# Kernel optimization log

Measured on AMD Instinct MI355X. Metric: run time of the kernel, lower is better.

Reference implementation:

```python
import jax, jax.numpy as jnp
import numpy as np

D_MODEL = 1024
N_HEADS = 16
D_K = D_MODEL // N_HEADS  # 64
SCALE = 0.125             # attention_scale = 1/sqrt(d_k)
ROPE_BASE = 10000.0
NEG_INF = -1e30


def setup_inputs() -> dict:
    key = jax.random.key(0)
    k1, k2, k3 = jax.random.split(key, 3)
    B, S = 2, 2048
    x = jax.random.normal(k1, (B, S, D_MODEL), jnp.float32)
    # torch Linear(d_model, 3*d_model, bias=False): stored here as [in, out]
    w_qkv = jax.random.normal(k2, (D_MODEL, 3 * D_MODEL), jnp.float32) * (D_MODEL ** -0.5)
    w_o = jax.random.normal(k3, (D_MODEL, D_MODEL), jnp.float32) * (D_MODEL ** -0.5)
    return {"x": x, "w_qkv": w_qkv, "w_o": w_o}


def _rotary(x):
    # x: [B, H, S, D]; standard half-split rotary over sequence positions
    S, D = x.shape[2], x.shape[3]
    inv_freq = 1.0 / (ROPE_BASE ** (jnp.arange(0, D, 2, dtype=jnp.float32) / D))  # [D/2]
    freqs = jnp.arange(S, dtype=jnp.float32)[:, None] * inv_freq[None, :]          # [S, D/2]
    cos = jnp.cos(freqs)[None, None]  # [1,1,S,D/2]
    sin = jnp.sin(freqs)[None, None]
    x1, x2 = jnp.split(x, 2, axis=-1)
    return jnp.concatenate([x1 * cos + x2 * sin, -x1 * sin + x2 * cos], axis=-1).astype(x.dtype)


def reference(x, w_qkv, w_o):
    B, S, _ = x.shape
    qkv = x @ w_qkv                                        # [B,S,3*D_MODEL]
    qkv = qkv.reshape(B, S, 3, N_HEADS, D_K).transpose(2, 0, 3, 1, 4)  # [3,B,H,S,Dk]
    q, k, v = qkv[0], qkv[1], qkv[2]
    q = _rotary(q)
    k = _rotary(k)
    scores = jnp.einsum('bhqd,bhkd->bhqk', q, k) * SCALE   # [B,H,S,S]
    causal = jnp.tril(jnp.ones((S, S), dtype=bool))
    scores = jnp.where(causal, scores, NEG_INF)
    attn = jax.nn.softmax(scores, axis=-1)
    out = jnp.einsum('bhqk,bhkd->bhqd', attn, v)           # [B,H,S,Dk]
    out = out.transpose(0, 2, 1, 3).reshape(B, S, D_MODEL)
    return out @ w_o
```

## Files before the change

### kernel.cpp

```cpp
#include <hip/hip_runtime.h>

typedef short bf16x8 __attribute__((ext_vector_type(8)));
typedef short bf16x4 __attribute__((ext_vector_type(4)));
typedef float f32x4 __attribute__((ext_vector_type(4)));
typedef float f32x16 __attribute__((ext_vector_type(16)));
typedef int i32x4 __attribute__((ext_vector_type(4)));

#define DEVI static __device__ __forceinline__

DEVI unsigned short f2b(float f) {
  unsigned u = __float_as_uint(f);
  u += 0x7FFFu + ((u >> 16) & 1u);
  return (unsigned short)(u >> 16);
}

DEVI void gload16(const void* g, void* l) {
  __builtin_amdgcn_global_load_lds((const __attribute__((address_space(1))) void*)g,
                                   (__attribute__((address_space(3))) void*)l, 16, 0, 0);
}

DEVI void pl32swap(int a, int b, int& outa, int& outb) {
#if __has_builtin(__builtin_amdgcn_permlane32_swap)
  auto r = __builtin_amdgcn_permlane32_swap(a, b, false, false);
  outa = ((const int*)&r)[0];
  outb = ((const int*)&r)[1];
#else
  int bp = __shfl_xor(b, 32);
  int ap = __shfl_xor(a, 32);
  outa = (threadIdx.x & 32) ? bp : a;
  outb = (threadIdx.x & 32) ? b : ap;
#endif
}

DEVI float halfmax(float x) {
  int o0, o1;
  pl32swap(__float_as_int(x), __float_as_int(x), o0, o1);
  return fmaxf(__int_as_float(o0), __int_as_float(o1));
}
DEVI float halfsum(float x) {
  int o0, o1;
  pl32swap(__float_as_int(x), __float_as_int(x), o0, o1);
  return __int_as_float(o0) + __int_as_float(o1);
}

__global__ void rope_table_kernel(float2* __restrict__ cst) {
  int i = blockIdx.x * 256 + threadIdx.x;
  int s = i >> 5, j = i & 31;
  float inv = powf(10000.0f, -(float)j * (1.0f / 32.0f));
  float a = (float)s * inv;
  cst[i] = make_float2(cosf(a), sinf(a));
}

__global__ void cvt_x_kernel(const float* __restrict__ x, unsigned short* __restrict__ xb) {
  int i = blockIdx.x * 256 + threadIdx.x;
  float4 v = ((const float4*)x)[i];
  ushort4 o;
  o.x = f2b(v.x); o.y = f2b(v.y); o.z = f2b(v.z); o.w = f2b(v.w);
  ((ushort4*)xb)[i] = o;
}

__global__ void transpose_kernel(const float* __restrict__ W, unsigned short* __restrict__ WT,
                                 int K, int N) {
  __shared__ float tile[32][33];
  int n0 = blockIdx.x * 32, k0 = blockIdx.y * 32;
  int tx = threadIdx.x, ty = threadIdx.y;
#pragma unroll
  for (int i = 0; i < 32; i += 8)
    tile[ty + i][tx] = W[(size_t)(k0 + ty + i) * N + n0 + tx];
  __syncthreads();
#pragma unroll
  for (int i = 0; i < 32; i += 8)
    WT[(size_t)(n0 + ty + i) * K + k0 + tx] = f2b(tile[tx][ty + i]);
}

__global__ __launch_bounds__(512, 2) void gemm_qkv_kernel(
    const unsigned short* __restrict__ Xb, const unsigned short* __restrict__ WT,
    const float2* __restrict__ cst,
    unsigned short* __restrict__ Qb, unsigned short* __restrict__ Kb,
    unsigned short* __restrict__ VTb) {
  __shared__ unsigned short As[2][256 * 64];
  __shared__ unsigned short Bs[2][256 * 64];
  const int tid = threadIdx.x;
  const int lane = tid & 63, wid = tid >> 6;
  const int flat = blockIdx.y * 12 + blockIdx.x;
  const int nf = (flat & 7) * 24 + (flat >> 3);
  const int bx = nf % 12, by = nf / 12;
  const int m0 = by * 256, n0 = bx * 256;
  const int wr = wid >> 2, wc = wid & 3;
  const int srow = lane >> 3;
  const int scc = ((lane & 7) ^ srow) * 8;
  const int rx = lane & 7;

  f32x4 acc[8][4] = {};

  auto stageA = [&](int k0, int nb, int i) {
    const int c = i * 8 + wid;
    const int row = c * 8 + srow;
    gload16(Xb + (size_t)(m0 + row) * 1024 + k0 + scc, (char*)As[nb] + c * 1024);
  };
  auto stageB = [&](int k0, int nb, int i) {
    const int c = i * 8 + wid;
    const int row = c * 8 + srow;
    gload16(WT + (size_t)(n0 + row) * 1024 + k0 + scc, (char*)Bs[nb] + c * 1024);
  };
  auto loadA = [&](const unsigned short* Ab, int q, bf16x8 af[2][2]) {
#pragma unroll
    for (int kk = 0; kk < 2; ++kk) {
      const int cc = ((kk * 4 + (lane >> 4)) ^ rx) * 8;
#pragma unroll
      for (int miL = 0; miL < 2; ++miL)
        af[miL][kk] = *(const bf16x8*)&Ab[(wr * 128 + (q * 2 + miL) * 16 + (lane & 15)) * 64 + cc];
    }
  };

#define QKV_MFMA_QUAD(Q)                                                      \
  __builtin_amdgcn_s_barrier();                                               \
  asm volatile("s_waitcnt lgkmcnt(0)" ::: "memory");                          \
  __builtin_amdgcn_s_setprio(1);                                              \
  _Pragma("unroll") for (int kk = 0; kk < 2; ++kk)                            \
    _Pragma("unroll") for (int miL = 0; miL < 2; ++miL)                       \
      _Pragma("unroll") for (int ni = 0; ni < 4; ++ni)                        \
        acc[(Q) * 2 + miL][ni] = __builtin_amdgcn_mfma_f32_16x16x32_bf16(     \
            af[miL][kk], bf[ni][kk], acc[(Q) * 2 + miL][ni], 0, 0, 0);        \
  __builtin_amdgcn_s_setprio(0);                                              \
  __builtin_amdgcn_s_barrier();

#pragma unroll
  for (int i = 0; i < 4; ++i) stageB(0, 0, i);
#pragma unroll
  for (int i = 0; i < 4; ++i) stageA(0, 0, i);
#pragma unroll
  for (int i = 0; i < 4; ++i) stageB(64, 1, i);
  stageA(64, 1, 0); stageA(64, 1, 2);
  asm volatile("s_waitcnt vmcnt(6)" ::: "memory");
  __builtin_amdgcn_s_barrier();

  for (int t = 0; t < 16; ++t) {
    const int b = t & 1;
    const unsigned short* Ab = As[b];
    const unsigned short* Bb = Bs[b];
    const int k1 = (t + 1) * 64, k2 = (t + 2) * 64;
    bf16x8 bf[4][2], af[2][2];

#pragma unroll
    for (int kk = 0; kk < 2; ++kk) {
      const int cc = ((kk * 4 + (lane >> 4)) ^ rx) * 8;
#pragma unroll
      for (int ni = 0; ni < 4; ++ni)
        bf[ni][kk] = *(const bf16x8*)&Bb[(wc * 64 + ni * 16 + (lane & 15)) * 64 + cc];
    }
    loadA(Ab, 0, af);
    if (t + 1 < 16) { stageA(k1, b ^ 1, 1); stageA(k1, b ^ 1, 3); }
    QKV_MFMA_QUAD(0)

    loadA(Ab, 1, af);
    if (t + 2 < 16) { stageB(k2, b, 0); stageB(k2, b, 1); }
    QKV_MFMA_QUAD(1)

    loadA(Ab, 2, af);
    if (t + 2 < 16) { stageB(k2, b, 2); stageB(k2, b, 3); }
    QKV_MFMA_QUAD(2)

    loadA(Ab, 3, af);
    if (t + 2 < 16) { stageA(k2, b, 0); stageA(k2, b, 2); }
    __builtin_amdgcn_s_barrier();
    asm volatile("s_waitcnt lgkmcnt(0)" ::: "memory");
    __builtin_amdgcn_s_setprio(1);
#pragma unroll
    for (int kk = 0; kk < 2; ++kk)
#pragma unroll
      for (int miL = 0; miL < 2; ++miL)
#pragma unroll
        for (int ni = 0; ni < 4; ++ni)
          acc[6 + miL][ni] = __builtin_amdgcn_mfma_f32_16x16x32_bf16(
              af[miL][kk], bf[ni][kk], acc[6 + miL][ni], 0, 0, 0);
    __builtin_amdgcn_s_setprio(0);
    if (t + 2 < 16) asm volatile("s_waitcnt vmcnt(6)" ::: "memory");
    else            asm volatile("s_waitcnt vmcnt(0)" ::: "memory");
    __builtin_amdgcn_s_barrier();
  }
#undef QKV_MFMA_QUAD

  unsigned short* slab = (wid < 4) ? (&As[0][0] + wid * 8192)
                                   : (&Bs[0][0] + (wid - 4) * 8192);
  const int n_base = n0 + wc * 64;
  const int ty = n_base >> 10;
  const int h = (n_base & 1023) >> 6;
  const int qrow = (lane >> 4) << 2;
  const int l15 = lane & 15;
  const int rlane = lane >> 3, clane = lane & 7;

  if (ty < 2) {
    unsigned short* dst = (ty == 0) ? Qb : Kb;
#pragma unroll
    for (int g = 0; g < 2; ++g) {
      const int rowg = m0 + wr * 128 + g * 64;
      const int s_half = rowg & 2047, bb = rowg >> 11;
#pragma unroll
      for (int miL = 0; miL < 4; ++miL) {
        const int mi = g * 4 + miL;
        const int rl0 = miL * 16 + qrow;
#pragma unroll
        for (int r = 0; r < 4; ++r) {
#pragma unroll
          for (int ni = 0; ni < 2; ++ni) {
            const int j = ni * 16 + l15;
            const float2 cs = cst[(s_half + rl0 + r) * 32 + j];
            const float x1 = acc[mi][ni][r], x2 = acc[mi][ni + 2][r];
            slab[(rl0 + r) * 72 + j]      = f2b(x1 * cs.x + x2 * cs.y);
            slab[(rl0 + r) * 72 + j + 32] = f2b(-x1 * cs.y + x2 * cs.x);
          }
        }
      }
      unsigned short* dp = dst + ((size_t)(bb * 16 + h) * 2048 + s_half) * 64;
#pragma unroll
      for (int i = 0; i < 8; ++i) {
        const int row = i * 8 + rlane;
        const bf16x8 v = *(const bf16x8*)&slab[row * 72 + clane * 8];
        *(bf16x8*)&dp[row * 64 + clane * 8] = v;
      }
    }
  } else {
#pragma unroll
    for (int g = 0; g < 2; ++g) {
      const int rowg = m0 + wr * 128 + g * 64;
      const int s_half = rowg & 2047, bb = rowg >> 11;
#pragma unroll
      for (int miL = 0; miL < 4; ++miL) {
        const int mi = g * 4 + miL;
        const int rl0 = miL * 16 + qrow;
#pragma unroll
        for (int ni = 0; ni < 4; ++ni) {
          const int d = ni * 16 + l15;
#pragma unroll
          for (int r = 0; r < 4; ++r)
            slab[d * 72 + rl0 + r] = f2b(acc[mi][ni][r]);
        }
      }
      unsigned short* vp = VTb + (size_t)(bb * 16 + h) * 64 * 2048 + s_half;
#pragma unroll
      for (int i = 0; i < 8; ++i) {
        const int d = i * 8 + rlane;
        const bf16x8 v = *(const bf16x8*)&slab[d * 72 + clane * 8];
        *(bf16x8*)&vp[(size_t)d * 2048 + clane * 8] = v;
      }
    }
  }
}

DEVI void gemm_mainloop(const unsigned short* __restrict__ A, const unsigned short* __restrict__ B,
                        unsigned short* As, unsigned short* Bs,
                        int m0, int n0, int lane, int wid, int wr, int wc,
                        f32x4 acc[4][4]) {
  const int srow = lane >> 3;
  const int scc = ((lane & 7) ^ srow) * 8;
  const int rx = lane & 7;
  auto stage = [&](int k0, int nb) {
    unsigned short* Ad = As + nb * 8192;
    unsigned short* Bd = Bs + nb * 8192;
#pragma unroll
    for (int i = 0; i < 4; ++i) {
      const int c = i * 4 + wid;
      const int row = c * 8 + srow;
      gload16(A + (size_t)(m0 + row) * 1024 + k0 + scc, (char*)Ad + c * 1024);
      gload16(B + (size_t)(n0 + row) * 1024 + k0 + scc, (char*)Bd + c * 1024);
    }
  };
  auto compute = [&](int nb) {
    const unsigned short* Ab = As + nb * 8192;
    const unsigned short* Bb = Bs + nb * 8192;
#pragma unroll
    for (int kk = 0; kk < 64; kk += 32) {
      const int cc = (((kk >> 3) + (lane >> 4)) ^ rx) * 8;
      bf16x8 a[4], b[4];
#pragma unroll
      for (int mi = 0; mi < 4; ++mi)
        a[mi] = *(const bf16x8*)&Ab[(wr * 64 + mi * 16 + (lane & 15)) * 64 + cc];
#pragma unroll
      for (int ni = 0; ni < 4; ++ni)
        b[ni] = *(const bf16x8*)&Bb[(wc * 64 + ni * 16 + (lane & 15)) * 64 + cc];
      __builtin_amdgcn_s_setprio(1);
#pragma unroll
      for (int mi = 0; mi < 4; ++mi)
#pragma unroll
        for (int ni = 0; ni < 4; ++ni)
          acc[mi][ni] = __builtin_amdgcn_mfma_f32_16x16x32_bf16(a[mi], b[ni], acc[mi][ni], 0, 0, 0);
      __builtin_amdgcn_s_setprio(0);
    }
  };
  stage(0, 0);
  stage(64, 1);
  for (int t = 0; t < 15; ++t) {
    asm volatile("s_waitcnt vmcnt(8)" ::: "memory");
    __builtin_amdgcn_s_barrier();
    compute(t & 1);
    __builtin_amdgcn_s_barrier();
    if (t < 14) stage((t + 2) * 64, t & 1);
  }
  asm volatile("s_waitcnt vmcnt(0)" ::: "memory");
  __builtin_amdgcn_s_barrier();
  compute(1);
}

DEVI void stage256(const unsigned short* __restrict__ Kh, const unsigned short* __restrict__ Vh,
                   int kbase, unsigned char* buf, int tid) {
#pragma unroll
  for (int i = 0; i < 4; ++i) {
    const int T = tid + i * 1024;
    const int g = T >> 10;
    const int rem = T & 1023;
    const int rr = (rem & 511) >> 3, c = rem & 7, cc = c ^ (rr & 7);
    unsigned char* dst = buf + (T & ~63) * 16;
    if (rem < 512)
      gload16(Kh + (size_t)(kbase + g * 64 + rr) * 64 + cc * 8, dst);
    else
      gload16(Vh + (size_t)rr * 2048 + kbase + g * 64 + cc * 8, dst);
  }
}

DEVI void attn_sub(const unsigned char* __restrict__ bufK, const unsigned char* __restrict__ bufV,
                   const bf16x8 qf[4], int s32, int kglob, bool diag, int qg, int ln, int hi,
                   float& m2, float& l_run, f32x16& acc0, f32x16& acc1) {
  const float C = 0.125f * 1.44269504f;
  const int rx = ln & 7;
  bf16x8 kf[4];
#pragma unroll
  for (int j = 0; j < 4; ++j) {
    const int cc = (2 * j + hi) ^ rx;
    kf[j] = *(const bf16x8*)(bufK + (s32 * 32 + ln) * 128 + cc * 16);
  }
  bf16x8 v0[2], v1[2];
#pragma unroll
  for (int p = 0; p < 2; ++p) {
    const int cc = (4 * s32 + 2 * p + hi) ^ rx;
    v0[p] = *(const bf16x8*)(bufV + ln * 128 + cc * 16);
    v1[p] = *(const bf16x8*)(bufV + (ln + 32) * 128 + cc * 16);
  }

  f32x16 stv = {};
  __builtin_amdgcn_s_setprio(1);
  stv = __builtin_amdgcn_mfma_f32_32x32x16_bf16(kf[0], qf[0], stv, 0, 0, 0);
  stv = __builtin_amdgcn_mfma_f32_32x32x16_bf16(kf[1], qf[1], stv, 0, 0, 0);
  stv = __builtin_amdgcn_mfma_f32_32x32x16_bf16(kf[2], qf[2], stv, 0, 0, 0);
  stv = __builtin_amdgcn_mfma_f32_32x32x16_bf16(kf[3], qf[3], stv, 0, 0, 0);
  __builtin_amdgcn_s_setprio(0);

  float sraw[16];
#pragma unroll
  for (int r = 0; r < 16; ++r) sraw[r] = stv[r];
  if (diag) {
#pragma unroll
    for (int r = 0; r < 16; ++r) {
      const int kg = kglob + (r & 3) + ((r >> 2) << 3) + (hi << 2);
      if (kg > qg) sraw[r] = -1e30f;
    }
  }
  float mraw = sraw[0];
#pragma unroll
  for (int r = 1; r < 16; ++r) mraw = fmaxf(mraw, sraw[r]);
  const float mlc = mraw * C;
  if (__any(mlc > m2 + 11.5416f)) {
    const float mnew = fmaxf(m2, halfmax(mlc));
    const float sc = exp2f(m2 - mnew);
    l_run *= sc;
#pragma unroll
    for (int r = 0; r < 16; ++r) { acc0[r] *= sc; acc1[r] *= sc; }
    m2 = mnew;
  }
  float p[16], ps = 0.f;
#pragma unroll
  for (int r = 0; r < 16; ++r) { p[r] = exp2f(fmaf(sraw[r], C, -m2)); ps += p[r]; }
  l_run += ps;

  int cw[8];
#pragma unroll
  for (int i = 0; i < 8; ++i)
    asm("v_cvt_pk_bf16_f32 %0, %1, %2" : "=v"(cw[i]) : "v"(p[2 * i]), "v"(p[2 * i + 1]));
  int a0, a1, b0, b1, a2, a3, b2, b3;
  pl32swap(cw[0], cw[2], a0, b0);
  pl32swap(cw[1], cw[3], a1, b1);
  pl32swap(cw[4], cw[6], a2, b2);
  pl32swap(cw[5], cw[7], a3, b3);
  const bf16x8 pa0 = __builtin_bit_cast(bf16x8, (i32x4){a0, a1, b0, b1});
  const bf16x8 pa1 = __builtin_bit_cast(bf16x8, (i32x4){a2, a3, b2, b3});

  __builtin_amdgcn_s_setprio(1);
  acc0 = __builtin_amdgcn_mfma_f32_32x32x16_bf16(v0[0], pa0, acc0, 0, 0, 0);
  acc0 = __builtin_amdgcn_mfma_f32_32x32x16_bf16(v0[1], pa1, acc0, 0, 0, 0);
  acc1 = __builtin_amdgcn_mfma_f32_32x32x16_bf16(v1[0], pa0, acc1, 0, 0, 0);
  acc1 = __builtin_amdgcn_mfma_f32_32x32x16_bf16(v1[1], pa1, acc1, 0, 0, 0);
  __builtin_amdgcn_s_setprio(0);
}

DEVI void write_partial(float* M, int slot, const f32x16& a0, const f32x16& a1,
                        float m2, float l) {
#pragma unroll
  for (int r = 0; r < 16; ++r) { M[slot + r] = a0[r]; M[slot + 16 + r] = a1[r]; }
  M[slot + 32] = m2;
  M[slot + 33] = l;
}

DEVI void merge_state(const float* M, int slot, float& m, float& l,
                      f32x16& a0, f32x16& a1) {
  const float mp = M[slot + 32], lp = M[slot + 33];
  const float mn = fmaxf(m, mp);
  const float eo = exp2f(m - mn), ep = exp2f(mp - mn);
  l = l * eo + lp * ep;
#pragma unroll
  for (int r = 0; r < 16; ++r) {
    a0[r] = a0[r] * eo + M[slot + r] * ep;
    a1[r] = a1[r] * eo + M[slot + 16 + r] * ep;
  }
  m = mn;
}

DEVI void writeO(unsigned short* __restrict__ Ob, const f32x16& a0, const f32x16& a1,
                 float l, int bh, int q0, int ln, int hi) {
  const float il = 1.0f / l;
  const int b = bh >> 4, h = bh & 15;
  unsigned short* ob = Ob + ((size_t)(b * 2048 + q0 + ln)) * 1024 + h * 64;
#pragma unroll
  for (int g = 0; g < 4; ++g) {
    ushort4 o0, o1;
    o0.x = f2b(a0[4 * g + 0] * il); o0.y = f2b(a0[4 * g + 1] * il);
    o0.z = f2b(a0[4 * g + 2] * il); o0.w = f2b(a0[4 * g + 3] * il);
    o1.x = f2b(a1[4 * g + 0] * il); o1.y = f2b(a1[4 * g + 1] * il);
    o1.z = f2b(a1[4 * g + 2] * il); o1.w = f2b(a1[4 * g + 3] * il);
    *(ushort4*)&ob[8 * g + 4 * hi]      = o0;
    *(ushort4*)&ob[32 + 8 * g + 4 * hi] = o1;
  }
}

__global__ __launch_bounds__(1024, 4) void attn_kernel(
    const unsigned short* __restrict__ Qb, const unsigned short* __restrict__ Kb,
    const unsigned short* __restrict__ VTb, unsigned short* __restrict__ Ob) {
  __shared__ unsigned char smem[2][65536];
  const int tid = threadIdx.x;
  const int lane = tid & 63, wid = tid >> 6;
  const int ln = lane & 31, hi = lane >> 5;
  const int s = wid & 3, qt = wid >> 2;
  const int bh = blockIdx.x;
  const int p = blockIdx.y;
  const int jA = 15 - p, jB = p;
  const unsigned short* Qh = Qb + (size_t)bh * 2048 * 64;
  const unsigned short* Kh = Kb + (size_t)bh * 2048 * 64;
  const unsigned short* Vh = VTb + (size_t)bh * 64 * 2048;
  const int rA = (2 * jA + 5) >> 2;
  const int rB = (2 * jB + 5) >> 2;

  auto load_q = [&](int q0, bf16x8 qf[4]) {
    const unsigned short* pq = Qh + (size_t)(q0 + ln) * 64 + hi * 8;
#pragma unroll
    for (int t = 0; t < 4; ++t) qf[t] = *(const bf16x8*)(pq + t * 16);
  };
  const int slot = (s * 64 + lane) * 34;
  int it = 0;

  {
    f32x16 a0 = {}, a1 = {};
    float m2 = -1e30f, l = 0.f;
    bf16x8 qf[4];
    load_q(jA * 128 + s * 32, qf);
    const int q0 = jA * 128 + s * 32, qg = q0 + ln, top = q0 >> 5;

    stage256(Kh, Vh, 0, &smem[0][0], tid);
    __syncthreads();
    for (int kb = 0; kb < rA; ++kb, ++it) {
      stage256(Kh, Vh, (kb + 1 < rA) ? (kb + 1) * 256 : 0, &smem[(it + 1) & 1][0], tid);
      const unsigned char* bufK = &smem[it & 1][0] + qt * 16384;
      const unsigned char* bufV = bufK + 8192;
      const int t64 = 4 * kb + qt;
#pragma unroll
      for (int s32 = 0; s32 < 2; ++s32) {
        const int g32 = 2 * t64 + s32;
        if (g32 <= top)
          attn_sub(bufK, bufV, qf, s32, g32 * 32, g32 == top, qg, ln, hi, m2, l, a0, a1);
      }
      __syncthreads();
    }
    l = halfsum(l);

    float* R = (float*)&smem[(rA + 1) & 1][0];
    if (qt == 1) write_partial(R, slot, a0, a1, m2, l);
    __syncthreads();
    if (qt == 0) merge_state(R, slot, m2, l, a0, a1);
    __syncthreads();
    if (qt == 3) write_partial(R, slot, a0, a1, m2, l);
    __syncthreads();
    if (qt == 2) merge_state(R, slot, m2, l, a0, a1);
    __syncthreads();
    if (qt == 2) write_partial(R, slot, a0, a1, m2, l);
    __syncthreads();
    if (qt == 0) merge_state(R, slot, m2, l, a0, a1);
    __syncthreads();
    if (qt == 0) writeO(Ob, a0, a1, l, bh, q0, ln, hi);
  }

  {
    f32x16 a0 = {}, a1 = {};
    float m2 = -1e30f, l = 0.f;
    bf16x8 qf[4];
    load_q(jB * 128 + s * 32, qf);
    const int q0 = jB * 128 + s * 32, qg = q0 + ln, top = q0 >> 5;

    for (int kb = 0; kb < rB; ++kb, ++it) {
      if (kb + 1 < rB) stage256(Kh, Vh, (kb + 1) * 256, &smem[(it + 1) & 1][0], tid);
      const unsigned char* bufK = &smem[it & 1][0] + qt * 16384;
      const unsigned char* bufV = bufK + 8192;
      const int t64 = 4 * kb + qt;
#pragma unroll
      for (int s32 = 0; s32 < 2; ++s32) {
        const int g32 = 2 * t64 + s32;
        if (g32 <= top)
          attn_sub(bufK, bufV, qf, s32, g32 * 32, g32 == top, qg, ln, hi, m2, l, a0, a1);
      }
      __syncthreads();
    }
    l = halfsum(l);

    float* R = (float*)&smem[0][0];
    if (qt == 1) write_partial(R, slot, a0, a1, m2, l);
    __syncthreads();
    if (qt == 0) merge_state(R, slot, m2, l, a0, a1);
    __syncthreads();
    if (qt == 3) write_partial(R, slot, a0, a1, m2, l);
    __syncthreads();
    if (qt == 2) merge_state(R, slot, m2, l, a0, a1);
    __syncthreads();
    if (qt == 2) write_partial(R, slot, a0, a1, m2, l);
    __syncthreads();
    if (qt == 0) {
      merge_state(R, slot, m2, l, a0, a1);
      writeO(Ob, a0, a1, l, bh, q0, ln, hi);
    }
  }
}

__global__ __launch_bounds__(256) void gemm_out_kernel(
    const unsigned short* __restrict__ Ob, const unsigned short* __restrict__ WoT,
    float* __restrict__ out) {
  __shared__ unsigned short As[2][128 * 64];
  __shared__ unsigned short Bs[2][128 * 64];
  const int lane = threadIdx.x & 63, wid = threadIdx.x >> 6;
  const int m0 = blockIdx.y * 128, n0 = blockIdx.x * 128;
  const int wr = wid >> 1, wc = wid & 1;
  f32x4 acc[4][4] = {};
  gemm_mainloop(Ob, WoT, &As[0][0], &Bs[0][0], m0, n0, lane, wid, wr, wc, acc);
#pragma unroll
  for (int mi = 0; mi < 4; ++mi) {
    const int mrow = m0 + wr * 64 + mi * 16 + ((lane >> 4) << 2);
#pragma unroll
    for (int ni = 0; ni < 4; ++ni) {
      const int n = n0 + wc * 64 + ni * 16 + (lane & 15);
#pragma unroll
      for (int r = 0; r < 4; ++r)
        out[(size_t)(mrow + r) * 1024 + n] = acc[mi][ni][r];
    }
  }
}

extern "C" void kernel_launch(void* const* d_in, const int* in_sizes, int n_in,
                              void* d_out, int out_size, void* d_ws, size_t ws_size,
                              hipStream_t stream) {
  const float* x     = (const float*)d_in[0];
  const float* w_qkv = (const float*)d_in[1];
  const float* w_o   = (const float*)d_in[2];
  float* out = (float*)d_out;
  char* ws = (char*)d_ws;

  const size_t MB = 1 << 20;
  float2* cst = (float2*)(ws);
  unsigned short* Xb  = (unsigned short*)(ws + (512 << 10));
  unsigned short* WqT = (unsigned short*)(ws + (512 << 10) + 8  * MB);
  unsigned short* WoT = (unsigned short*)(ws + (512 << 10) + 14 * MB);
  unsigned short* Qb  = (unsigned short*)(ws + (512 << 10) + 16 * MB);
  unsigned short* Kb  = (unsigned short*)(ws + (512 << 10) + 24 * MB);
  unsigned short* VTb = (unsigned short*)(ws + (512 << 10) + 32 * MB);
  unsigned short* Ob  = Xb;

  rope_table_kernel<<<dim3(256), dim3(256), 0, stream>>>(cst);
  cvt_x_kernel<<<dim3(4096), dim3(256), 0, stream>>>(x, Xb);
  transpose_kernel<<<dim3(96, 32), dim3(32, 8), 0, stream>>>(w_qkv, WqT, 1024, 3072);
  transpose_kernel<<<dim3(32, 32), dim3(32, 8), 0, stream>>>(w_o, WoT, 1024, 1024);
  gemm_qkv_kernel<<<dim3(12, 16), dim3(512), 0, stream>>>(Xb, WqT, cst, Qb, Kb, VTb);
  attn_kernel<<<dim3(32, 8), dim3(1024), 0, stream>>>(Qb, Kb, VTb, Ob);
  gemm_out_kernel<<<dim3(8, 32), dim3(256), 0, stream>>>(Ob, WoT, out);
}
```

Baseline: 120.7 us.

## Replace 256x256 QKV GEMM with 128x128 tiles using shared mainloop

Drops the hand-scheduled 256x256-tile, 512-thread QKV projection GEMM and reuses the generic 128x128 double-buffered mainloop from the output projection, launched on a 24x32 grid of 256-thread blocks. The fused RoPE and V-transpose epilogue is adapted to the smaller per-warp 64x64 tiles. The goal is more blocks (768 instead of 192) for better CU occupancy and load balance on the 256-CU part. The cost is lower operand reuse per tile, which means more global and LDS traffic, and the loss of the interleaved prefetch schedule.

```diff
diff --git a/kernel.cpp b/kernel.cpp
--- a/kernel.cpp
+++ b/kernel.cpp
@@ -73,181 +73,6 @@
     WT[(size_t)(n0 + ty + i) * K + k0 + tx] = f2b(tile[tx][ty + i]);
 }
 
-__global__ __launch_bounds__(512, 2) void gemm_qkv_kernel(
-    const unsigned short* __restrict__ Xb, const unsigned short* __restrict__ WT,
-    const float2* __restrict__ cst,
-    unsigned short* __restrict__ Qb, unsigned short* __restrict__ Kb,
-    unsigned short* __restrict__ VTb) {
-  __shared__ unsigned short As[2][256 * 64];
-  __shared__ unsigned short Bs[2][256 * 64];
-  const int tid = threadIdx.x;
-  const int lane = tid & 63, wid = tid >> 6;
-  const int flat = blockIdx.y * 12 + blockIdx.x;
-  const int nf = (flat & 7) * 24 + (flat >> 3);
-  const int bx = nf % 12, by = nf / 12;
-  const int m0 = by * 256, n0 = bx * 256;
-  const int wr = wid >> 2, wc = wid & 3;
-  const int srow = lane >> 3;
-  const int scc = ((lane & 7) ^ srow) * 8;
-  const int rx = lane & 7;
-
-  f32x4 acc[8][4] = {};
-
-  auto stageA = [&](int k0, int nb, int i) {
-    const int c = i * 8 + wid;
-    const int row = c * 8 + srow;
-    gload16(Xb + (size_t)(m0 + row) * 1024 + k0 + scc, (char*)As[nb] + c * 1024);
-  };
-  auto stageB = [&](int k0, int nb, int i) {
-    const int c = i * 8 + wid;
-    const int row = c * 8 + srow;
-    gload16(WT + (size_t)(n0 + row) * 1024 + k0 + scc, (char*)Bs[nb] + c * 1024);
-  };
-  auto loadA = [&](const unsigned short* Ab, int q, bf16x8 af[2][2]) {
-#pragma unroll
-    for (int kk = 0; kk < 2; ++kk) {
-      const int cc = ((kk * 4 + (lane >> 4)) ^ rx) * 8;
-#pragma unroll
-      for (int miL = 0; miL < 2; ++miL)
-        af[miL][kk] = *(const bf16x8*)&Ab[(wr * 128 + (q * 2 + miL) * 16 + (lane & 15)) * 64 + cc];
-    }
-  };
-
-#define QKV_MFMA_QUAD(Q)                                                      \
-  __builtin_amdgcn_s_barrier();                                               \
-  asm volatile("s_waitcnt lgkmcnt(0)" ::: "memory");                          \
-  __builtin_amdgcn_s_setprio(1);                                              \
-  _Pragma("unroll") for (int kk = 0; kk < 2; ++kk)                            \
-    _Pragma("unroll") for (int miL = 0; miL < 2; ++miL)                       \
-      _Pragma("unroll") for (int ni = 0; ni < 4; ++ni)                        \
-        acc[(Q) * 2 + miL][ni] = __builtin_amdgcn_mfma_f32_16x16x32_bf16(     \
-            af[miL][kk], bf[ni][kk], acc[(Q) * 2 + miL][ni], 0, 0, 0);        \
-  __builtin_amdgcn_s_setprio(0);                                              \
-  __builtin_amdgcn_s_barrier();
-
-#pragma unroll
-  for (int i = 0; i < 4; ++i) stageB(0, 0, i);
-#pragma unroll
-  for (int i = 0; i < 4; ++i) stageA(0, 0, i);
-#pragma unroll
-  for (int i = 0; i < 4; ++i) stageB(64, 1, i);
-  stageA(64, 1, 0); stageA(64, 1, 2);
-  asm volatile("s_waitcnt vmcnt(6)" ::: "memory");
-  __builtin_amdgcn_s_barrier();
-
-  for (int t = 0; t < 16; ++t) {
-    const int b = t & 1;
-    const unsigned short* Ab = As[b];
-    const unsigned short* Bb = Bs[b];
-    const int k1 = (t + 1) * 64, k2 = (t + 2) * 64;
-    bf16x8 bf[4][2], af[2][2];
-
-#pragma unroll
-    for (int kk = 0; kk < 2; ++kk) {
-      const int cc = ((kk * 4 + (lane >> 4)) ^ rx) * 8;
-#pragma unroll
-      for (int ni = 0; ni < 4; ++ni)
-        bf[ni][kk] = *(const bf16x8*)&Bb[(wc * 64 + ni * 16 + (lane & 15)) * 64 + cc];
-    }
-    loadA(Ab, 0, af);
-    if (t + 1 < 16) { stageA(k1, b ^ 1, 1); stageA(k1, b ^ 1, 3); }
-    QKV_MFMA_QUAD(0)
-
-    loadA(Ab, 1, af);
-    if (t + 2 < 16) { stageB(k2, b, 0); stageB(k2, b, 1); }
-    QKV_MFMA_QUAD(1)
-
-    loadA(Ab, 2, af);
-    if (t + 2 < 16) { stageB(k2, b, 2); stageB(k2, b, 3); }
-    QKV_MFMA_QUAD(2)
-
-    loadA(Ab, 3, af);
-    if (t + 2 < 16) { stageA(k2, b, 0); stageA(k2, b, 2); }
-    __builtin_amdgcn_s_barrier();
-    asm volatile("s_waitcnt lgkmcnt(0)" ::: "memory");
-    __builtin_amdgcn_s_setprio(1);
-#pragma unroll
-    for (int kk = 0; kk < 2; ++kk)
-#pragma unroll
-      for (int miL = 0; miL < 2; ++miL)
-#pragma unroll
-        for (int ni = 0; ni < 4; ++ni)
-          acc[6 + miL][ni] = __builtin_amdgcn_mfma_f32_16x16x32_bf16(
-              af[miL][kk], bf[ni][kk], acc[6 + miL][ni], 0, 0, 0);
-    __builtin_amdgcn_s_setprio(0);
-    if (t + 2 < 16) asm volatile("s_waitcnt vmcnt(6)" ::: "memory");
-    else            asm volatile("s_waitcnt vmcnt(0)" ::: "memory");
-    __builtin_amdgcn_s_barrier();
-  }
-#undef QKV_MFMA_QUAD
-
-  unsigned short* slab = (wid < 4) ? (&As[0][0] + wid * 8192)
-                                   : (&Bs[0][0] + (wid - 4) * 8192);
-  const int n_base = n0 + wc * 64;
-  const int ty = n_base >> 10;
-  const int h = (n_base & 1023) >> 6;
-  const int qrow = (lane >> 4) << 2;
-  const int l15 = lane & 15;
-  const int rlane = lane >> 3, clane = lane & 7;
-
-  if (ty < 2) {
-    unsigned short* dst = (ty == 0) ? Qb : Kb;
-#pragma unroll
-    for (int g = 0; g < 2; ++g) {
-      const int rowg = m0 + wr * 128 + g * 64;
-      const int s_half = rowg & 2047, bb = rowg >> 11;
-#pragma unroll
-      for (int miL = 0; miL < 4; ++miL) {
-        const int mi = g * 4 + miL;
-        const int rl0 = miL * 16 + qrow;
-#pragma unroll
-        for (int r = 0; r < 4; ++r) {
-#pragma unroll
-          for (int ni = 0; ni < 2; ++ni) {
-            const int j = ni * 16 + l15;
-            const float2 cs = cst[(s_half + rl0 + r) * 32 + j];
-            const float x1 = acc[mi][ni][r], x2 = acc[mi][ni + 2][r];
-            slab[(rl0 + r) * 72 + j]      = f2b(x1 * cs.x + x2 * cs.y);
-            slab[(rl0 + r) * 72 + j + 32] = f2b(-x1 * cs.y + x2 * cs.x);
-          }
-        }
-      }
-      unsigned short* dp = dst + ((size_t)(bb * 16 + h) * 2048 + s_half) * 64;
-#pragma unroll
-      for (int i = 0; i < 8; ++i) {
-        const int row = i * 8 + rlane;
-        const bf16x8 v = *(const bf16x8*)&slab[row * 72 + clane * 8];
-        *(bf16x8*)&dp[row * 64 + clane * 8] = v;
-      }
-    }
-  } else {
-#pragma unroll
-    for (int g = 0; g < 2; ++g) {
-      const int rowg = m0 + wr * 128 + g * 64;
-      const int s_half = rowg & 2047, bb = rowg >> 11;
-#pragma unroll
-      for (int miL = 0; miL < 4; ++miL) {
-        const int mi = g * 4 + miL;
-        const int rl0 = miL * 16 + qrow;
-#pragma unroll
-        for (int ni = 0; ni < 4; ++ni) {
-          const int d = ni * 16 + l15;
-#pragma unroll
-          for (int r = 0; r < 4; ++r)
-            slab[d * 72 + rl0 + r] = f2b(acc[mi][ni][r]);
-        }
-      }
-      unsigned short* vp = VTb + (size_t)(bb * 16 + h) * 64 * 2048 + s_half;
-#pragma unroll
-      for (int i = 0; i < 8; ++i) {
-        const int d = i * 8 + rlane;
-        const bf16x8 v = *(const bf16x8*)&slab[d * 72 + clane * 8];
-        *(bf16x8*)&vp[(size_t)d * 2048 + clane * 8] = v;
-      }
-    }
-  }
-}
-
 DEVI void gemm_mainloop(const unsigned short* __restrict__ A, const unsigned short* __restrict__ B,
                         unsigned short* As, unsigned short* Bs,
                         int m0, int n0, int lane, int wid, int wr, int wc,
@@ -300,6 +125,79 @@
   asm volatile("s_waitcnt vmcnt(0)" ::: "memory");
   __builtin_amdgcn_s_barrier();
   compute(1);
+}
+
+__global__ __launch_bounds__(256, 2) void gemm_qkv_kernel(
+    const unsigned short* __restrict__ Xb, const unsigned short* __restrict__ WT,
+    const float2* __restrict__ cst,
+    unsigned short* __restrict__ Qb, unsigned short* __restrict__ Kb,
+    unsigned short* __restrict__ VTb) {
+  __shared__ unsigned short As[2][8192];
+  __shared__ unsigned short Bs[2][8192];
+  const int lane = threadIdx.x & 63, wid = threadIdx.x >> 6;
+  const int flat = blockIdx.y * 24 + blockIdx.x;
+  const int nf = (flat & 7) * 96 + (flat >> 3);
+  const int bx = nf % 24, by = nf / 24;
+  const int m0 = by * 128, n0 = bx * 128;
+  const int wr = wid >> 1, wc = wid & 1;
+  f32x4 acc[4][4] = {};
+  gemm_mainloop(Xb, WT, &As[0][0], &Bs[0][0], m0, n0, lane, wid, wr, wc, acc);
+
+  __syncthreads();
+  unsigned short* slab = (unsigned short*)((char*)&As[0][0] + wid * 9216);
+  const int n_base = n0 + wc * 64;
+  const int ty = n_base >> 10;
+  const int h = (n_base & 1023) >> 6;
+  const int qrow = (lane >> 4) << 2;
+  const int l15 = lane & 15;
+  const int rlane = lane >> 3, clane = lane & 7;
+  const int rowg = m0 + wr * 64;
+  const int s_half = rowg & 2047, bb = rowg >> 11;
+
+  if (ty < 2) {
+    unsigned short* dst = (ty == 0) ? Qb : Kb;
+#pragma unroll
+    for (int mi = 0; mi < 4; ++mi) {
+      const int rl0 = mi * 16 + qrow;
+#pragma unroll
+      for (int r = 0; r < 4; ++r) {
+#pragma unroll
+        for (int ni = 0; ni < 2; ++ni) {
+          const int j = ni * 16 + l15;
+          const float2 cs = cst[(s_half + rl0 + r) * 32 + j];
+          const float x1 = acc[mi][ni][r], x2 = acc[mi][ni + 2][r];
+          slab[(rl0 + r) * 72 + j]      = f2b(x1 * cs.x + x2 * cs.y);
+          slab[(rl0 + r) * 72 + j + 32] = f2b(-x1 * cs.y + x2 * cs.x);
+        }
+      }
+    }
+    unsigned short* dp = dst + ((size_t)(bb * 16 + h) * 2048 + s_half) * 64;
+#pragma unroll
+    for (int i = 0; i < 8; ++i) {
+      const int row = i * 8 + rlane;
+      const bf16x8 v = *(const bf16x8*)&slab[row * 72 + clane * 8];
+      *(bf16x8*)&dp[row * 64 + clane * 8] = v;
+    }
+  } else {
+#pragma unroll
+    for (int mi = 0; mi < 4; ++mi) {
+      const int rl0 = mi * 16 + qrow;
+#pragma unroll
+      for (int ni = 0; ni < 4; ++ni) {
+        const int d = ni * 16 + l15;
+#pragma unroll
+        for (int r = 0; r < 4; ++r)
+          slab[d * 72 + rl0 + r] = f2b(acc[mi][ni][r]);
+      }
+    }
+    unsigned short* vp = VTb + (size_t)(bb * 16 + h) * 64 * 2048 + s_half;
+#pragma unroll
+    for (int i = 0; i < 8; ++i) {
+      const int d = i * 8 + rlane;
+      const bf16x8 v = *(const bf16x8*)&slab[d * 72 + clane * 8];
+      *(bf16x8*)&vp[(size_t)d * 2048 + clane * 8] = v;
+    }
+  }
 }
 
 DEVI void stage256(const unsigned short* __restrict__ Kh, const unsigned short* __restrict__ Vh,
@@ -539,8 +437,8 @@
 __global__ __launch_bounds__(256) void gemm_out_kernel(
     const unsigned short* __restrict__ Ob, const unsigned short* __restrict__ WoT,
     float* __restrict__ out) {
-  __shared__ unsigned short As[2][128 * 64];
-  __shared__ unsigned short Bs[2][128 * 64];
+  __shared__ unsigned short As[2][8192];
+  __shared__ unsigned short Bs[2][8192];
   const int lane = threadIdx.x & 63, wid = threadIdx.x >> 6;
   const int m0 = blockIdx.y * 128, n0 = blockIdx.x * 128;
   const int wr = wid >> 1, wc = wid & 1;
@@ -582,7 +480,7 @@
   cvt_x_kernel<<<dim3(4096), dim3(256), 0, stream>>>(x, Xb);
   transpose_kernel<<<dim3(96, 32), dim3(32, 8), 0, stream>>>(w_qkv, WqT, 1024, 3072);
   transpose_kernel<<<dim3(32, 32), dim3(32, 8), 0, stream>>>(w_o, WoT, 1024, 1024);
-  gemm_qkv_kernel<<<dim3(12, 16), dim3(512), 0, stream>>>(Xb, WqT, cst, Qb, Kb, VTb);
+  gemm_qkv_kernel<<<dim3(24, 32), dim3(256), 0, stream>>>(Xb, WqT, cst, Qb, Kb, VTb);
   attn_kernel<<<dim3(32, 8), dim3(1024), 0, stream>>>(Qb, Kb, VTb, Ob);
   gemm_out_kernel<<<dim3(8, 32), dim3(256), 0, stream>>>(Ob, WoT, out);
 }
```

After: 121.1 us. Within noise of the previous version (+0.4%).
